# Optimization experiments

Measured on AMD Instinct MI355X. Metric: run time of the kernel, lower is better.

## Reference

```python
import jax, jax.numpy as jnp
import numpy as np

N = 20000; E = 320000; IN = 128; OUT = 128; H = 8; D = 16
SQRT_DK = float(D) ** 0.5

def setup_inputs() -> dict:
    key = jax.random.key(0)
    ks = jax.random.split(key, 20)
    s = 0.05
    glorot = (6.0 / (D + D)) ** 0.5
    inp = dict(
        h_a=jax.random.normal(ks[0], (N, IN), jnp.float32),
        h_b=jax.random.normal(ks[1], (N, IN), jnp.float32),
        Wk=jax.random.normal(ks[2], (2, IN, OUT), jnp.float32) * s,
        bk=jnp.zeros((2, OUT), jnp.float32),
        Wq=jax.random.normal(ks[3], (2, IN, OUT), jnp.float32) * s,
        bq=jnp.zeros((2, OUT), jnp.float32),
        Wv=jax.random.normal(ks[4], (2, IN, OUT), jnp.float32) * s,
        bv=jnp.zeros((2, OUT), jnp.float32),
        Wa=jax.random.normal(ks[5], (2, OUT, OUT), jnp.float32) * s,
        ba=jnp.zeros((2, OUT), jnp.float32),
        rel_att=jax.random.normal(ks[6], (4, H, D, D), jnp.float32) * glorot,
        rel_msg=jax.random.normal(ks[7], (4, H, D, D), jnp.float32) * glorot,
        rel_pri=jnp.ones((4, H), jnp.float32),
        skip=jnp.ones((2,), jnp.float32),
    )
    names = ["src_aa", "dst_aa", "src_ab", "dst_ab", "src_ba", "dst_ba", "src_bb", "dst_bb"]
    for i, name in enumerate(names):
        inp[name] = jax.random.randint(ks[8 + i], (E,), 0, N, jnp.int32)
    return inp

def _relation(h_src, h_dst, src, dst, Wk_t, bk_t, Wq_t, bq_t, Wv_t, bv_t, att, msg, pri):
    # relation-specific K/V transform + Q projection
    k = (h_src @ Wk_t + bk_t).reshape(-1, H, D)
    v = (h_src @ Wv_t + bv_t).reshape(-1, H, D)
    q = (h_dst @ Wq_t + bq_t).reshape(-1, H, D)
    k = jnp.einsum('nhd,hde->nhe', k, att)
    v = jnp.einsum('nhd,hde->nhe', v, msg)
    # edge dot-product score (v_dot_u: q[dst] . k[src]), [E, H]
    score = jnp.einsum('ehd,ehd->eh', q[dst], k[src]) * pri / SQRT_DK
    # edge softmax normalized by dst
    smax = jax.ops.segment_max(score, dst, num_segments=N)
    ex = jnp.exp(score - smax[dst])
    ssum = jax.ops.segment_sum(ex, dst, num_segments=N)
    attn = ex / ssum[dst]
    # weighted scatter-aggregate, [N, H, D]
    return jax.ops.segment_sum(v[src] * attn[:, :, None], dst, num_segments=N)

def reference(h_a, h_b, Wk, bk, Wq, bq, Wv, bv, Wa, ba, rel_att, rel_msg, rel_pri, skip,
              src_aa, dst_aa, src_ab, dst_ab, src_ba, dst_ba, src_bb, dst_bb):
    agg_aa = _relation(h_a, h_a, src_aa, dst_aa, Wk[0], bk[0], Wq[0], bq[0], Wv[0], bv[0], rel_att[0], rel_msg[0], rel_pri[0])
    agg_ab = _relation(h_a, h_b, src_ab, dst_ab, Wk[0], bk[0], Wq[1], bq[1], Wv[0], bv[0], rel_att[1], rel_msg[1], rel_pri[1])
    agg_ba = _relation(h_b, h_a, src_ba, dst_ba, Wk[1], bk[1], Wq[0], bq[0], Wv[1], bv[1], rel_att[2], rel_msg[2], rel_pri[2])
    agg_bb = _relation(h_b, h_b, src_bb, dst_bb, Wk[1], bk[1], Wq[1], bq[1], Wv[1], bv[1], rel_att[3], rel_msg[3], rel_pri[3])
    # cross_reducer='mean' over the 2 relations targeting each node type
    t_a = (0.5 * (agg_aa + agg_ba)).reshape(N, OUT)
    t_b = (0.5 * (agg_ab + agg_bb)).reshape(N, OUT)
    al_a = jax.nn.sigmoid(skip[0])
    al_b = jax.nn.sigmoid(skip[1])
    new_a = al_a * (t_a @ Wa[0] + ba[0]) + (1.0 - al_a) * h_a
    new_b = al_b * (t_b @ Wa[1] + ba[1]) + (1.0 - al_b) * h_b
    return new_a, new_b
```

## Files before the change

### kernel.cpp

```cpp
#include <hip/hip_runtime.h>
#include <stdint.h>

#define N_NODES 20000
#define N_EDGES 320000
#define C 128
#define H 8
#define D 16
#define SLOT 64
#define NRANGE 5000
#define RANGES2 10000
#define CAP2 80

#define P_CVT 2500
#define P_ZERO 625
#define P_PACK 128
#define P_FUSE 32
#define MB_TOTAL 8130

typedef short s16x8 __attribute__((ext_vector_type(8)));
typedef float f32x4 __attribute__((ext_vector_type(4)));

__device__ __forceinline__ unsigned short f2bf(float f) {
    unsigned int b = __float_as_uint(f);
    b += 0x7fffu + ((b >> 16) & 1u);
    return (unsigned short)(b >> 16);
}
__device__ __forceinline__ float bf2f(unsigned int u) {
    return __uint_as_float(u << 16);
}

__global__ __launch_bounds__(256) void prep_k(const float* __restrict__ h_a, const float* __restrict__ h_b,
                                              unsigned short* __restrict__ oa, unsigned short* __restrict__ ob,
                                              const float* __restrict__ Wq, const float* __restrict__ Wa,
                                              unsigned short* __restrict__ Wqt, unsigned short* __restrict__ Wat,
                                              const float* __restrict__ Wk, const float* __restrict__ Wv,
                                              const float* __restrict__ bk, const float* __restrict__ bv,
                                              const float* __restrict__ att, const float* __restrict__ msg,
                                              unsigned short* __restrict__ Wkt, unsigned short* __restrict__ Wvt,
                                              float* __restrict__ bkt, float* __restrict__ bvt,
                                              int* __restrict__ cur) {
    __shared__ float sa[D * D], sm[D * D];
    int bid = blockIdx.x;
    int tid = threadIdx.x;
    if (bid < P_CVT) {
        int i = (bid * 256 + tid) * 4;
        float4 va = *(const float4*)(h_a + i);
        float4 vb = *(const float4*)(h_b + i);
        ushort4 ua = { f2bf(va.x), f2bf(va.y), f2bf(va.z), f2bf(va.w) };
        ushort4 ub = { f2bf(vb.x), f2bf(vb.y), f2bf(vb.z), f2bf(vb.w) };
        *(ushort4*)(oa + i) = ua;
        *(ushort4*)(ob + i) = ub;
        return;
    }
    bid -= P_CVT;
    if (bid < P_ZERO) {
        int i = bid * 256 + tid;
        if (i < 160000) ((int4*)cur)[i] = make_int4(0, 0, 0, 0);
        return;
    }
    bid -= P_ZERO;
    if (bid < P_PACK) {
        int n = bid;
        int t = tid >> 7, i = tid & 127;
        Wqt[(t * C + n) * C + i] = f2bf(Wq[(t * C + i) * C + n]);
        Wat[(t * C + n) * C + i] = f2bf(Wa[(t * C + i) * C + n]);
        return;
    }
    bid -= P_PACK;
    {
        int r = bid >> 3, h = bid & 7;
        int t = r >> 1;
        if (tid < D * D) {
            sa[tid] = att[(r * H + h) * D * D + tid];
            sm[tid] = msg[(r * H + h) * D * D + tid];
        }
        __syncthreads();
        int i = tid & 127;
        for (int e = (tid >> 7); e < D; e += 2) {
            float sk = 0.f, sv = 0.f;
            for (int d = 0; d < D; ++d) {
                sk += Wk[(t * C + i) * C + h * D + d] * sa[d * D + e];
                sv += Wv[(t * C + i) * C + h * D + d] * sm[d * D + e];
            }
            Wkt[(r * C + h * D + e) * C + i] = f2bf(sk);
            Wvt[(r * C + h * D + e) * C + i] = f2bf(sv);
        }
        if (tid < D) {
            int e = tid;
            float sk = 0.f, sv = 0.f;
            for (int d = 0; d < D; ++d) {
                sk += bk[t * C + h * D + d] * sa[d * D + e];
                sv += bv[t * C + h * D + d] * sm[d * D + e];
            }
            bkt[r * C + h * D + e] = sk;
            bvt[r * C + h * D + e] = sv;
        }
    }
}

__global__ __launch_bounds__(256) void mega_k(const int* __restrict__ s0, const int* __restrict__ s1,
                                              const int* __restrict__ s2, const int* __restrict__ s3,
                                              const int* __restrict__ d0, const int* __restrict__ d1,
                                              const int* __restrict__ d2, const int* __restrict__ d3,
                                              int* __restrict__ cur, unsigned short* __restrict__ part,
                                              const unsigned short* __restrict__ ha,
                                              const unsigned short* __restrict__ hb,
                                              const unsigned short* __restrict__ Wqt,
                                              const unsigned short* __restrict__ Wkt,
                                              const unsigned short* __restrict__ Wvt,
                                              const float* __restrict__ bq,
                                              const float* __restrict__ bkt,
                                              const float* __restrict__ bvt,
                                              unsigned short* __restrict__ Qa,
                                              unsigned short* __restrict__ Qb,
                                              unsigned short* __restrict__ Kall,
                                              unsigned short* __restrict__ Vall) {
    int bid = blockIdx.x;
    int part_id = -1, proj_id = -1;
    if (bid < 8125) {
        int p = bid / 13, o = bid - p * 13;
        if (o < 8) part_id = p * 8 + o;
        else       proj_id = p * 5 + (o - 8);
    } else {
        proj_id = 3125 + (bid - 8125);
    }

    if (part_id >= 0) {
        int r = part_id / 1250;
        int eb = part_id - r * 1250;
        int e = eb * 256 + threadIdx.x;
        const int* dd = (r == 0) ? d0 : (r == 1) ? d1 : (r == 2) ? d2 : d3;
        const int* ss = (r == 0) ? s0 : (r == 1) ? s1 : (r == 2) ? s2 : s3;
        int d = dd[e];
        int range = d >> 1;
        int pos = atomicAdd(&cur[(r * RANGES2 + range) * 16], 1);
        if (pos < CAP2)
            part[((size_t)(r * RANGES2 + range)) * CAP2 + pos] =
                (unsigned short)(ss[e] | ((d & 1) << 15));
        return;
    }
    int j = proj_id / 313;
    int xb = proj_id - j * 313;
    const unsigned short* A;
    const unsigned short* Wt;
    const float* bias;
    unsigned short* Out;
    if (j < 2) {
        A = j ? hb : ha; Wt = Wqt + j * C * C; bias = bq + j * C; Out = j ? Qb : Qa;
    } else if (j < 6) {
        int r = j - 2;
        A = (r < 2) ? ha : hb; Wt = Wkt + r * C * C; bias = bkt + r * C;
        Out = Kall + (size_t)r * N_NODES * C;
    } else {
        int r = j - 6;
        A = (r < 2) ? ha : hb; Wt = Wvt + r * C * C; bias = bvt + r * C;
        Out = Vall + (size_t)r * N_NODES * C;
    }
    int wid = threadIdx.x >> 6, l = threadIdx.x & 63;
    int row_base = xb * 64 + wid * 16;
    int lm = l & 15, q = l >> 4;
    f32x4 acc[8] = {};
    int arow = row_base + lm;
    if (arow >= N_NODES) arow = N_NODES - 1;
    const s16x8* Ap = (const s16x8*)(A + (size_t)arow * C);
#pragma unroll
    for (int kc = 0; kc < 4; ++kc) {
        s16x8 af = Ap[kc * 4 + q];
#pragma unroll
        for (int t = 0; t < 8; ++t) {
            s16x8 bf = *(const s16x8*)(Wt + (t * 16 + lm) * C + kc * 32 + q * 8);
            acc[t] = __builtin_amdgcn_mfma_f32_16x16x32_bf16(af, bf, acc[t], 0, 0, 0);
        }
    }
#pragma unroll
    for (int t = 0; t < 8; ++t) {
        int col = t * 16 + lm;
        float b = bias[col];
#pragma unroll
        for (int i = 0; i < 4; ++i) {
            int row = row_base + q * 4 + i;
            if (row < N_NODES) Out[(size_t)row * C + col] = f2bf(acc[t][i] + b);
        }
    }
}

__global__ __launch_bounds__(256) void final_mm(const unsigned short* __restrict__ AggAll,
                                                const unsigned short* __restrict__ WatAll,
                                                const float* __restrict__ baAll,
                                                const float* __restrict__ skip,
                                                const float* __restrict__ h_a,
                                                const float* __restrict__ h_b,
                                                float* __restrict__ OutAll) {
    int ty = blockIdx.y;
    const unsigned short* Agg = AggAll + (size_t)ty * N_NODES * C;
    const unsigned short* Wat = WatAll + ty * C * C;
    const float* ba = baAll + ty * C;
    const float* h_orig = ty ? h_b : h_a;
    float* Out = OutAll + (size_t)ty * N_NODES * C;
    int wid = threadIdx.x >> 6, l = threadIdx.x & 63;
    int row_base = blockIdx.x * 64 + wid * 16;
    int lm = l & 15, q = l >> 4;
    f32x4 acc[8] = {};
    int arow = row_base + lm;
    if (arow >= N_NODES) arow = N_NODES - 1;
    const s16x8* Ap = (const s16x8*)(Agg + (size_t)arow * C);
#pragma unroll
    for (int kc = 0; kc < 4; ++kc) {
        s16x8 af = Ap[kc * 4 + q];
#pragma unroll
        for (int t = 0; t < 8; ++t) {
            s16x8 bf = *(const s16x8*)(Wat + (t * 16 + lm) * C + kc * 32 + q * 8);
            acc[t] = __builtin_amdgcn_mfma_f32_16x16x32_bf16(af, bf, acc[t], 0, 0, 0);
        }
    }
    float al = 1.f / (1.f + __expf(-skip[ty]));
#pragma unroll
    for (int t = 0; t < 8; ++t) {
        int col = t * 16 + lm;
        float b = ba[col];
#pragma unroll
        for (int i = 0; i < 4; ++i) {
            int row = row_base + q * 4 + i;
            if (row < N_NODES)
                Out[(size_t)row * C + col] = al * (acc[t][i] + b) + (1.f - al) * h_orig[(size_t)row * C + col];
        }
    }
}

__global__ __launch_bounds__(256) void node_p2(const int* __restrict__ cur,
                                               const unsigned short* __restrict__ part,
                                               const unsigned int* __restrict__ Kall,
                                               const unsigned int* __restrict__ Vall,
                                               const float* __restrict__ pri,
                                               const unsigned int* __restrict__ Qa,
                                               const unsigned int* __restrict__ Qb,
                                               unsigned int* __restrict__ agg) {
    __shared__ unsigned short slot[2][4][SLOT];
    __shared__ int cnt[2][4];
    int g = blockIdx.x;
    int type = (g >= NRANGE) ? 1 : 0;
    int range = g - type * NRANGE;
    int relA = type ? 1 : 0;
    int relB = type ? 3 : 2;
    if (threadIdx.x < 8) ((int*)cnt)[threadIdx.x] = 0;
    __syncthreads();
#pragma unroll
    for (int rr = 0; rr < 2; ++rr) {
        int rel = rr ? relB : relA;
#pragma unroll
        for (int seg = 0; seg < 2; ++seg) {
            int r2 = range * 2 + seg;
            int c = cur[(rel * RANGES2 + r2) * 16];
            if (c > CAP2) c = CAP2;
            const unsigned short* pp = part + ((size_t)(rel * RANGES2 + r2)) * CAP2;
            for (int i = threadIdx.x; i < c; i += 256) {
                unsigned int rec = pp[i];
                int dof = 2 * seg + (rec >> 15);
                int p = atomicAdd(&cnt[rr][dof], 1);
                if (p < SLOT) slot[rr][dof][p] = (unsigned short)(rec & 0x7fffu);
            }
        }
    }
    __syncthreads();

    int wid = threadIdx.x >> 6, l = threadIdx.x & 63;
    int hg = l >> 3;
    int dof = wid;
    int n = range * 4 + dof;
    const unsigned int* Q32 = type ? Qb : Qa;
    unsigned int qv = Q32[(size_t)n * 64 + l];
    float q0 = bf2f(qv & 0xffffu), q1 = bf2f(qv >> 16);
    float outx = 0.f, outy = 0.f;

#pragma unroll 1
    for (int rr = 0; rr < 2; ++rr) {
        int rel = rr ? relB : relA;
        const unsigned int* K32 = Kall + (size_t)rel * N_NODES * 64;
        const unsigned int* V32 = Vall + (size_t)rel * N_NODES * 64;
        float pv = pri[rel * 8 + hg] * 0.25f;
        int deg = cnt[rr][dof];
        if (deg > SLOT) deg = SLOT;
        float m = -1e30f, sum = 0.f;
        float ax0 = 0.f, ay0 = 0.f, ax1 = 0.f, ay1 = 0.f;
        for (int base = 0; base < deg; base += 16) {
            int cc = deg - base;
            if (cc > 16) cc = 16;
            float s[16];
            unsigned int vv[16];
#pragma unroll
            for (int i = 0; i < 16; ++i) {
                float d = -1e30f;
                unsigned int v = 0;
                if (i < cc) {
                    int sv = slot[rr][dof][base + i];
                    unsigned int kv = K32[(size_t)sv * 64 + l];
                    v = V32[(size_t)sv * 64 + l];
                    d = q0 * bf2f(kv & 0xffffu) + q1 * bf2f(kv >> 16);
                    d += __shfl_xor(d, 1);
                    d += __shfl_xor(d, 2);
                    d += __shfl_xor(d, 4);
                    d *= pv;
                }
                s[i] = d;
                vv[i] = v;
            }
            float mloc = s[0];
#pragma unroll
            for (int i = 1; i < 16; ++i) mloc = fmaxf(mloc, s[i]);
            float mnew = fmaxf(m, mloc);
            float alpha = __expf(m - mnew);
            sum *= alpha; ax0 *= alpha; ay0 *= alpha; ax1 *= alpha; ay1 *= alpha;
            m = mnew;
#pragma unroll
            for (int i = 0; i < 16; i += 2) {
                if (i < cc) {
                    float ww = __expf(s[i] - m);
                    sum += ww;
                    ax0 += ww * bf2f(vv[i] & 0xffffu);
                    ay0 += ww * bf2f(vv[i] >> 16);
                }
                if (i + 1 < cc) {
                    float ww = __expf(s[i + 1] - m);
                    sum += ww;
                    ax1 += ww * bf2f(vv[i + 1] & 0xffffu);
                    ay1 += ww * bf2f(vv[i + 1] >> 16);
                }
            }
        }
        if (deg > 0) {
            float rs = 1.f / sum;
            outx += (ax0 + ax1) * rs;
            outy += (ay0 + ay1) * rs;
        }
    }
    unsigned int packed = (unsigned int)f2bf(0.5f * outx) | ((unsigned int)f2bf(0.5f * outy) << 16);
    agg[((size_t)type * N_NODES + n) * 64 + l] = packed;
}

extern "C" void kernel_launch(void* const* d_in, const int* in_sizes, int n_in,
                              void* d_out, int out_size, void* d_ws, size_t ws_size,
                              hipStream_t stream) {
    const float* h_a  = (const float*)d_in[0];
    const float* h_b  = (const float*)d_in[1];
    const float* Wk   = (const float*)d_in[2];
    const float* bk   = (const float*)d_in[3];
    const float* Wq   = (const float*)d_in[4];
    const float* bq   = (const float*)d_in[5];
    const float* Wv   = (const float*)d_in[6];
    const float* bv   = (const float*)d_in[7];
    const float* Wa   = (const float*)d_in[8];
    const float* ba   = (const float*)d_in[9];
    const float* att  = (const float*)d_in[10];
    const float* msg  = (const float*)d_in[11];
    const float* pri  = (const float*)d_in[12];
    const float* skip = (const float*)d_in[13];
    const int* srcs[4] = {(const int*)d_in[14], (const int*)d_in[16], (const int*)d_in[18], (const int*)d_in[20]};
    const int* dsts[4] = {(const int*)d_in[15], (const int*)d_in[17], (const int*)d_in[19], (const int*)d_in[21]};
    float* out = (float*)d_out;

    char* w = (char*)d_ws;
    auto alloc = [&](size_t bytes) {
        char* p = w;
        w += (bytes + 255) & ~(size_t)255;
        return p;
    };
    unsigned short* ha_bf = (unsigned short*)alloc((size_t)N_NODES * C * 2);
    unsigned short* hb_bf = (unsigned short*)alloc((size_t)N_NODES * C * 2);
    unsigned short* Qa    = (unsigned short*)alloc((size_t)N_NODES * C * 2);
    unsigned short* Qb    = (unsigned short*)alloc((size_t)N_NODES * C * 2);
    unsigned short* Kall  = (unsigned short*)alloc((size_t)4 * N_NODES * C * 2);
    unsigned short* Vall  = (unsigned short*)alloc((size_t)4 * N_NODES * C * 2);
    unsigned short* Wqt   = (unsigned short*)alloc(2 * C * C * 2);
    unsigned short* Wat   = (unsigned short*)alloc(2 * C * C * 2);
    unsigned short* Wkt   = (unsigned short*)alloc(4 * C * C * 2);
    unsigned short* Wvt   = (unsigned short*)alloc(4 * C * C * 2);
    float* bkt            = (float*)alloc(4 * C * 4);
    float* bvt            = (float*)alloc(4 * C * 4);
    int* cur              = (int*)alloc(4 * RANGES2 * 16 * 4);
    unsigned short* part  = (unsigned short*)alloc((size_t)4 * RANGES2 * CAP2 * 2);
    unsigned short* agg   = (unsigned short*)alloc((size_t)2 * N_NODES * C * 2);

    prep_k<<<P_CVT + P_ZERO + P_PACK + P_FUSE, 256, 0, stream>>>(
        h_a, h_b, ha_bf, hb_bf, Wq, Wa, Wqt, Wat,
        Wk, Wv, bk, bv, att, msg, Wkt, Wvt, bkt, bvt, cur);

    mega_k<<<MB_TOTAL, 256, 0, stream>>>(
        srcs[0], srcs[1], srcs[2], srcs[3],
        dsts[0], dsts[1], dsts[2], dsts[3],
        cur, part,
        ha_bf, hb_bf, Wqt, Wkt, Wvt, bq, bkt, bvt,
        Qa, Qb, Kall, Vall);

    node_p2<<<2 * NRANGE, 256, 0, stream>>>(cur, part,
                                            (const unsigned int*)Kall, (const unsigned int*)Vall,
                                            pri,
                                            (const unsigned int*)Qa, (const unsigned int*)Qb,
                                            (unsigned int*)agg);

    final_mm<<<dim3(313, 2), 256, 0, stream>>>(agg, Wat, ba, skip, h_a, h_b, out);
}
```

Measured before the change: 349.7 us.

## Process four edges per wavefront with 16-byte K/V loads in attention aggregation

The edge-softmax aggregation kernel now splits each 64-lane wavefront into four 16-lane groups. Each group handles a different edge, and each lane loads 16 bytes (8 bf16 values) of K and V instead of 4 bytes. Each group keeps its own online-softmax state, and the four partial max, sum and accumulator values are merged with cross-lane shuffles at the end. The aim is fewer, wider memory transactions, shorter shuffle reductions and fewer serial iterations per destination node, at the cost of more registers per lane and an extra merge step.

```diff
diff --git a/kernel.cpp b/kernel.cpp
--- a/kernel.cpp
+++ b/kernel.cpp
@@ -27,6 +27,12 @@
 }
 __device__ __forceinline__ float bf2f(unsigned int u) {
     return __uint_as_float(u << 16);
+}
+__device__ __forceinline__ float bf_lo(unsigned int u) {
+    return __uint_as_float(u << 16);
+}
+__device__ __forceinline__ float bf_hi(unsigned int u) {
+    return __uint_as_float(u & 0xffff0000u);
 }
 
 __global__ __launch_bounds__(256) void prep_k(const float* __restrict__ h_a, const float* __restrict__ h_b,
@@ -264,77 +270,93 @@
     __syncthreads();
 
     int wid = threadIdx.x >> 6, l = threadIdx.x & 63;
-    int hg = l >> 3;
+    int eg = l >> 4;
+    int j  = l & 15;
+    int hg = j >> 1;
     int dof = wid;
     int n = range * 4 + dof;
     const unsigned int* Q32 = type ? Qb : Qa;
-    unsigned int qv = Q32[(size_t)n * 64 + l];
-    float q0 = bf2f(qv & 0xffffu), q1 = bf2f(qv >> 16);
-    float outx = 0.f, outy = 0.f;
+    uint4 qv = *(const uint4*)(Q32 + (size_t)n * 64 + j * 4);
+    float q0 = bf_lo(qv.x), q1 = bf_hi(qv.x), q2 = bf_lo(qv.y), q3 = bf_hi(qv.y);
+    float q4 = bf_lo(qv.z), q5 = bf_hi(qv.z), q6 = bf_lo(qv.w), q7 = bf_hi(qv.w);
+    float out[8] = {};
 
 #pragma unroll 1
     for (int rr = 0; rr < 2; ++rr) {
         int rel = rr ? relB : relA;
-        const unsigned int* K32 = Kall + (size_t)rel * N_NODES * 64;
-        const unsigned int* V32 = Vall + (size_t)rel * N_NODES * 64;
+        const char* Kb = (const char*)(Kall + (size_t)rel * N_NODES * 64);
+        const char* Vb = (const char*)(Vall + (size_t)rel * N_NODES * 64);
         float pv = pri[rel * 8 + hg] * 0.25f;
         int deg = cnt[rr][dof];
         if (deg > SLOT) deg = SLOT;
         float m = -1e30f, sum = 0.f;
-        float ax0 = 0.f, ay0 = 0.f, ax1 = 0.f, ay1 = 0.f;
+        float acc[8] = {};
         for (int base = 0; base < deg; base += 16) {
-            int cc = deg - base;
-            if (cc > 16) cc = 16;
-            float s[16];
-            unsigned int vv[16];
-#pragma unroll
-            for (int i = 0; i < 16; ++i) {
+            float s[4];
+            uint4 vv[4];
+#pragma unroll
+            for (int i = 0; i < 4; ++i) {
+                int idx = base + i * 4 + eg;
                 float d = -1e30f;
-                unsigned int v = 0;
-                if (i < cc) {
-                    int sv = slot[rr][dof][base + i];
-                    unsigned int kv = K32[(size_t)sv * 64 + l];
-                    v = V32[(size_t)sv * 64 + l];
-                    d = q0 * bf2f(kv & 0xffffu) + q1 * bf2f(kv >> 16);
+                uint4 v = {0u, 0u, 0u, 0u};
+                if (idx < deg) {
+                    unsigned off = ((unsigned)slot[rr][dof][idx] << 8) | ((unsigned)j << 4);
+                    uint4 kv = *(const uint4*)(Kb + off);
+                    v = *(const uint4*)(Vb + off);
+                    d = q0 * bf_lo(kv.x) + q1 * bf_hi(kv.x)
+                      + q2 * bf_lo(kv.y) + q3 * bf_hi(kv.y)
+                      + q4 * bf_lo(kv.z) + q5 * bf_hi(kv.z)
+                      + q6 * bf_lo(kv.w) + q7 * bf_hi(kv.w);
                     d += __shfl_xor(d, 1);
-                    d += __shfl_xor(d, 2);
-                    d += __shfl_xor(d, 4);
                     d *= pv;
                 }
                 s[i] = d;
                 vv[i] = v;
             }
-            float mloc = s[0];
-#pragma unroll
-            for (int i = 1; i < 16; ++i) mloc = fmaxf(mloc, s[i]);
+            float mloc = fmaxf(fmaxf(s[0], s[1]), fmaxf(s[2], s[3]));
             float mnew = fmaxf(m, mloc);
             float alpha = __expf(m - mnew);
-            sum *= alpha; ax0 *= alpha; ay0 *= alpha; ax1 *= alpha; ay1 *= alpha;
+            sum *= alpha;
+#pragma unroll
+            for (int c2 = 0; c2 < 8; ++c2) acc[c2] *= alpha;
             m = mnew;
 #pragma unroll
-            for (int i = 0; i < 16; i += 2) {
-                if (i < cc) {
-                    float ww = __expf(s[i] - m);
-                    sum += ww;
-                    ax0 += ww * bf2f(vv[i] & 0xffffu);
-                    ay0 += ww * bf2f(vv[i] >> 16);
-                }
-                if (i + 1 < cc) {
-                    float ww = __expf(s[i + 1] - m);
-                    sum += ww;
-                    ax1 += ww * bf2f(vv[i + 1] & 0xffffu);
-                    ay1 += ww * bf2f(vv[i + 1] >> 16);
-                }
+            for (int i = 0; i < 4; ++i) {
+                float ww = (s[i] > -1e29f) ? __expf(s[i] - m) : 0.f;
+                sum += ww;
+                acc[0] += ww * bf_lo(vv[i].x); acc[1] += ww * bf_hi(vv[i].x);
+                acc[2] += ww * bf_lo(vv[i].y); acc[3] += ww * bf_hi(vv[i].y);
+                acc[4] += ww * bf_lo(vv[i].z); acc[5] += ww * bf_hi(vv[i].z);
+                acc[6] += ww * bf_lo(vv[i].w); acc[7] += ww * bf_hi(vv[i].w);
             }
+        }
+        float m1 = fmaxf(m, __shfl_xor(m, 16));
+        float m2 = fmaxf(m1, __shfl_xor(m1, 32));
+        float beta = __expf(m - m2);
+        sum *= beta;
+        sum += __shfl_xor(sum, 16);
+        sum += __shfl_xor(sum, 32);
+#pragma unroll
+        for (int c2 = 0; c2 < 8; ++c2) {
+            float a = acc[c2] * beta;
+            a += __shfl_xor(a, 16);
+            a += __shfl_xor(a, 32);
+            acc[c2] = a;
         }
         if (deg > 0) {
             float rs = 1.f / sum;
-            outx += (ax0 + ax1) * rs;
-            outy += (ay0 + ay1) * rs;
-        }
-    }
-    unsigned int packed = (unsigned int)f2bf(0.5f * outx) | ((unsigned int)f2bf(0.5f * outy) << 16);
-    agg[((size_t)type * N_NODES + n) * 64 + l] = packed;
+#pragma unroll
+            for (int c2 = 0; c2 < 8; ++c2) out[c2] += acc[c2] * rs;
+        }
+    }
+    if (eg == 0) {
+        uint4 pk;
+        pk.x = (unsigned int)f2bf(0.5f * out[0]) | ((unsigned int)f2bf(0.5f * out[1]) << 16);
+        pk.y = (unsigned int)f2bf(0.5f * out[2]) | ((unsigned int)f2bf(0.5f * out[3]) << 16);
+        pk.z = (unsigned int)f2bf(0.5f * out[4]) | ((unsigned int)f2bf(0.5f * out[5]) << 16);
+        pk.w = (unsigned int)f2bf(0.5f * out[6]) | ((unsigned int)f2bf(0.5f * out[7]) << 16);
+        *(uint4*)(agg + ((size_t)type * N_NODES + n) * 64 + j * 4) = pk;
+    }
 }
 
 extern "C" void kernel_launch(void* const* d_in, const int* in_sizes, int n_in,
```

After: 319.7 us. -8.6%, faster.
